# Performance work log

Measured on AMD Instinct MI355X. Metric: run time of the kernel, lower is better.

## Reference

```python
import jax, jax.numpy as jnp
import numpy as np

B, T, C = 2, 512, 128
H = 4 * C
EPS_LN = 1e-5
EPS_WKV = 1e-6


def setup_inputs() -> dict:
    key = jax.random.key(0)
    ks = jax.random.split(key, 12)
    def rn(i, shape, s):
        return jax.random.normal(ks[i], shape, jnp.float32) * s
    return {
        "x": jax.random.normal(ks[0], (B, T, C), jnp.float32),
        "ln1_g": jnp.ones((C,), jnp.float32), "ln1_b": jnp.zeros((C,), jnp.float32),
        "mu": rn(1, (C,), 0.1),
        "Wr": rn(2, (C, C), 0.02), "br": jnp.zeros((C,), jnp.float32),
        "Wk": rn(3, (C, C), 0.02), "bk": jnp.zeros((C,), jnp.float32),
        "Wv": rn(4, (C, C), 0.02), "bv": jnp.zeros((C,), jnp.float32),
        "w_decay": rn(5, (C,), 0.5),
        "Wo": rn(6, (C, C), 0.02), "bo": jnp.zeros((C,), jnp.float32),
        "ln2_g": jnp.ones((C,), jnp.float32), "ln2_b": jnp.zeros((C,), jnp.float32),
        "W1": rn(7, (C, H), 0.02), "b1": jnp.zeros((H,), jnp.float32),
        "W2": rn(8, (H, C), 0.02), "b2": jnp.zeros((C,), jnp.float32),
    }


def _ln(x, g, b):
    m = x.mean(-1, keepdims=True)
    v = ((x - m) ** 2).mean(-1, keepdims=True)
    return (x - m) * jax.lax.rsqrt(v + EPS_LN) * g + b


def _wkv_dir(k, v, w_lc):
    # k, v: (B,T,C); w_lc: (T,C) per-(position,channel) decay weight
    p = k[:, :, None, :] * w_lc[None, None, :, :]              # (B,T,L,C)
    p = jnp.exp(p - jax.lax.stop_gradient(p.max(-1, keepdims=True)))  # stable, max over C (as in source, dim=-1)
    p = p / (p.sum(-1, keepdims=True) + EPS_WKV)               # normalize over channel dim, as written in torch
    return jnp.einsum('btlc,blc->btc', p, v)


def _forward(x, ln1_g, ln1_b, mu, Wr, br, Wk, bk, Wv, bv, w_decay, Wo, bo, ln2_g, ln2_b, W1, b1, W2, b2):
    Tn = x.shape[1]
    h = _ln(x, ln1_g, ln1_b)
    # TemporalShift: past half shifted right, future half shifted left
    xp, xf = jnp.split(h, 2, axis=-1)
    xp = jnp.pad(xp, ((0, 0), (1, 0), (0, 0)))[:, :-1]
    xf = jnp.pad(xf, ((0, 0), (0, 1), (0, 0)))[:, 1:]
    hs = h + mu * jnp.concatenate([xp, xf], axis=-1)
    r = jax.nn.sigmoid(hs @ Wr + br)
    k = hs @ Wk + bk
    v = hs @ Wv + bv
    t = jnp.arange(Tn, dtype=x.dtype)[:, None]                 # (T,1)
    neg_w = -jnp.exp(w_decay)[None, :]                         # (1,C)
    w_f = neg_w * (Tn - 1 - t) / (Tn - 1)                      # (T,C)
    w_b = neg_w * t / (Tn - 1)                                 # (T,C)
    x_f = _wkv_dir(k, v, w_f)
    x_b = jnp.flip(_wkv_dir(jnp.flip(k, 1), jnp.flip(v, 1), w_b), 1)
    wk = r * (x_f + x_b) * 0.5
    y = x + wk @ Wo + bo
    h2 = _ln(y, ln2_g, ln2_b)
    m = jax.nn.gelu(h2 @ W1 + b1, approximate=False) @ W2 + b2
    return y + m


def reference(x, ln1_g, ln1_b, mu, Wr, br, Wk, bk, Wv, bv, w_decay, Wo, bo, ln2_g, ln2_b, W1, b1, W2, b2):
    return _forward(x, ln1_g, ln1_b, mu, Wr, br, Wk, bk, Wv, bv, w_decay, Wo, bo, ln2_g, ln2_b, W1, b1, W2, b2)
```

## Files before the change

### kernel.cpp

```cpp
#include <hip/hip_runtime.h>
#include <hip/hip_bf16.h>

#define Bq 2
#define Tq 512
#define Cq 128
#define Hq 512
#define NROW (Bq*Tq)

__device__ __forceinline__ float bfbits2f(unsigned short u) {
    return __uint_as_float(((unsigned)u) << 16);
}
__device__ __forceinline__ bool detect_f32(const void* sent) {
    return *(const unsigned*)sent == 0x3F800000u;
}
#define LD(p, i) (f32 ? ((const float*)(p))[i] : bfbits2f(((const unsigned short*)(p))[i]))
__device__ __forceinline__ float4 LD4(const void* p, int i, bool f32) {
    if (f32) return ((const float4*)p)[i >> 2];
    ushort4 u = *(const ushort4*)((const unsigned short*)p + i);
    return make_float4(bfbits2f(u.x), bfbits2f(u.y), bfbits2f(u.z), bfbits2f(u.w));
}

__global__ __launch_bounds__(512) void kA_qkv(
    const void* __restrict__ sent,
    const void* __restrict__ x,
    const void* __restrict__ ln1g, const void* __restrict__ ln1b,
    const void* __restrict__ mu,
    const void* __restrict__ Wr, const void* __restrict__ br,
    const void* __restrict__ Wk, const void* __restrict__ bk,
    const void* __restrict__ Wv, const void* __restrict__ bv,
    const void* __restrict__ wdec,
    float* __restrict__ r_out, float* __restrict__ u_out,
    float* __restrict__ v_out)
{
    const bool f32 = detect_f32(sent);
    int R0 = blockIdx.x * 2, tid = threadIdx.x;
    int g = tid >> 7, col = tid & 127;
    int t0 = R0 & (Tq - 1);
    int bbase = R0 - t0;

    __shared__ float h4[4][Cq];
    __shared__ __align__(16) float hsi[Cq][2];
    __shared__ __align__(16) float partA[3][2][2][Cq];
    __shared__ float wred[8][2];

    {
        int t = t0 - 1 + g;
        int tcl = min(max(t, 0), Tq - 1);
        int row = bbase + tcl;
        float xv = LD(x, row * Cq + col);
        float s1 = xv, s2 = xv * xv;
        for (int off = 32; off; off >>= 1) {
            s1 += __shfl_xor(s1, off);
            s2 += __shfl_xor(s2, off);
        }
        int wid = tid >> 6;
        if ((tid & 63) == 0) { wred[wid][0] = s1; wred[wid][1] = s2; }
        __syncthreads();
        float S1 = wred[2 * g][0] + wred[2 * g + 1][0];
        float S2 = wred[2 * g][1] + wred[2 * g + 1][1];
        float m  = S1 * (1.f / Cq);
        float va = S2 * (1.f / Cq) - m * m;
        float rs = rsqrtf(va + 1e-5f);
        h4[g][col] = (xv - m) * rs * LD(ln1g, col) + LD(ln1b, col);
    }
    __syncthreads();

    if (g < 2) {
        int r2 = g, tt = t0 + r2;
        float hv = h4[r2 + 1][col];
        float nb;
        if (col < Cq / 2) nb = (tt > 0)      ? h4[r2][col]     : 0.f;
        else              nb = (tt < Tq - 1) ? h4[r2 + 2][col] : 0.f;
        hsi[col][r2] = hv + LD(mu, col) * nb;
    }
    __syncthreads();

    {
        int w = tid >> 6, lane = tid & 63;
        if (w < 6) {
            int m = w >> 1, kh = w & 1;
            const void* W = (m == 0) ? Wr : (m == 1) ? Wk : Wv;
            int ks2 = lane >> 5, j0 = (lane & 31) * 4;
            int cbase = kh * 64 + ks2 * 32;
            float a00 = 0.f, a01 = 0.f, a02 = 0.f, a03 = 0.f;
            float a10 = 0.f, a11 = 0.f, a12 = 0.f, a13 = 0.f;
#pragma unroll 4
            for (int cc = cbase; cc < cbase + 32; ++cc) {
                float4 wv = LD4(W, cc * Cq + j0, f32);
                float2 hv = *(const float2*)&hsi[cc][0];
                a00 += hv.x * wv.x; a01 += hv.x * wv.y; a02 += hv.x * wv.z; a03 += hv.x * wv.w;
                a10 += hv.y * wv.x; a11 += hv.y * wv.y; a12 += hv.y * wv.z; a13 += hv.y * wv.w;
            }
            a00 += __shfl_xor(a00, 32);
            a01 += __shfl_xor(a01, 32);
            a02 += __shfl_xor(a02, 32);
            a03 += __shfl_xor(a03, 32);
            a10 += __shfl_xor(a10, 32);
            a11 += __shfl_xor(a11, 32);
            a12 += __shfl_xor(a12, 32);
            a13 += __shfl_xor(a13, 32);
            if (ks2 == 0) {
                *(float4*)&partA[m][kh][0][j0] = make_float4(a00, a01, a02, a03);
                *(float4*)&partA[m][kh][1][j0] = make_float4(a10, a11, a12, a13);
            }
        }
    }
    __syncthreads();

    if (g < 3) {
        int m = g;
        float ar0 = partA[m][0][0][col] + partA[m][1][0][col];
        float ar1 = partA[m][0][1][col] + partA[m][1][1][col];
        if (m == 0) {
            float bb = LD(br, col);
            r_out[(R0 + 0) * Cq + col] = 1.f / (1.f + __expf(-(ar0 + bb)));
            r_out[(R0 + 1) * Cq + col] = 1.f / (1.f + __expf(-(ar1 + bb)));
        } else if (m == 1) {
            float bb = LD(bk, col);
            float wd = LD(wdec, col);
            wd = fminf(fmaxf(wd, -20.f), 20.f);
            float negw = -__expf(wd);
            float u0 = (ar0 + bb) * negw;
            float u1 = (ar1 + bb) * negw;
            u0 = fminf(fmaxf(u0, -30.f), 30.f);
            u1 = fminf(fmaxf(u1, -30.f), 30.f);
            u_out[(R0 + 0) * Cq + col] = u0;
            u_out[(R0 + 1) * Cq + col] = u1;
        } else {
            float bb = LD(bv, col);
            v_out[(R0 + 0) * Cq + col] = ar0 + bb;
            v_out[(R0 + 1) * Cq + col] = ar1 + bb;
        }
    }
}

__global__ __launch_bounds__(512) void kB_wkv_ffn(
    const void* __restrict__ sent,
    const float* __restrict__ u_in,
    const float* __restrict__ v_in,
    const float* __restrict__ r_in,
    const void* __restrict__ x,
    const void* __restrict__ Wo, const void* __restrict__ bo,
    const void* __restrict__ lng, const void* __restrict__ lnb,
    const void* __restrict__ W1, const void* __restrict__ b1,
    const void* __restrict__ W2, const void* __restrict__ b2,
    void* __restrict__ out)
{
    const bool f32 = detect_f32(sent);
    int R0 = blockIdx.x * 2, tid = threadIdx.x;
    int b = R0 >> 9;
    const float inv511 = 1.f / (float)(Tq - 1);
    int w = tid >> 6, lane = tid & 63;

    __shared__ float u2[2][Cq];
    __shared__ __align__(16) float rinv2[Tq][2];
    __shared__ float part[8][2][Cq];
    __shared__ __align__(16) float wki[Cq][2];
    __shared__ __align__(16) float h2i[Cq][2];
    __shared__ __align__(16) float m1i[Hq][2];
    __shared__ __align__(16) float pbuf[16 * Cq * 2];
    __shared__ float wred[8][2];

    {
        const float4* us = (const float4*)(u_in + (size_t)R0 * Cq);
        ((float4*)u2)[lane] = us[lane];
    }
    float rv_pre = 0.f, xv_pre = 0.f;
    if (tid < 256) {
        int r = tid >> 7, c = tid & 127;
        rv_pre = r_in[(R0 + r) * Cq + c];
        xv_pre = LD(x, (R0 + r) * Cq + c);
    }

    {
        int l = (Tq - 1) - tid;
        float a = (float)tid * inv511 * 1.44269504f;
#pragma unroll
        for (int r = 0; r < 2; ++r) {
            float s0 = 0.f, s1 = 0.f, s2 = 0.f, s3 = 0.f;
            const float4* uu4 = (const float4*)u2[r];
            for (int cc = 0; cc < Cq / 4; ++cc) {
                float4 uv = uu4[cc];
                s0 += exp2f(a * uv.x);
                s1 += exp2f(a * uv.y);
                s2 += exp2f(a * uv.z);
                s3 += exp2f(a * uv.w);
            }
            rinv2[l][r] = 1.f / ((s0 + s1) + (s2 + s3) + 1e-6f);
        }
    }

    {
        int c2 = lane * 2;
        float u00 = u2[0][c2], u01 = u2[0][c2 + 1];
        float u10 = u2[1][c2], u11 = u2[1][c2 + 1];
        int j0 = w * 64;
        float jb = (float)j0;
        float e00 = __expf(u00 * jb * inv511), e01 = __expf(u01 * jb * inv511);
        float e10 = __expf(u10 * jb * inv511), e11 = __expf(u11 * jb * inv511);
        float g00 = __expf(u00 * inv511), g01 = __expf(u01 * inv511);
        float g10 = __expf(u10 * inv511), g11 = __expf(u11 * inv511);
        float a00 = 0.f, a01 = 0.f, a10 = 0.f, a11 = 0.f;
        int lhi = (Tq - 1) - j0;
        const float2* vp = (const float2*)(v_in + (size_t)b * Tq * Cq) + lane + (size_t)lhi * 64;
        const float2* rp = (const float2*)rinv2 + lhi;
        float2 v0 = vp[0], v1 = vp[-64], v2 = vp[-128], v3 = vp[-192];

#define WKV_QUAD(r0_, r1_, r2_, r3_)                                          \
        {                                                                     \
            { float f1 = e00 * g00, f2 = f1 * g00, f3 = f2 * g00;             \
              a00 += v0.x * (e00 * r0_.x);                                    \
              a00 += v1.x * (f1 * r1_.x);                                     \
              a00 += v2.x * (f2 * r2_.x);                                     \
              a00 += v3.x * (f3 * r3_.x);                                     \
              e00 = f3 * g00; }                                               \
            { float f1 = e01 * g01, f2 = f1 * g01, f3 = f2 * g01;             \
              a01 += v0.y * (e01 * r0_.x);                                    \
              a01 += v1.y * (f1 * r1_.x);                                    \
              a01 += v2.y * (f2 * r2_.x);                                    \
              a01 += v3.y * (f3 * r3_.x);                                    \
              e01 = f3 * g01; }                                               \
            { float f1 = e10 * g10, f2 = f1 * g10, f3 = f2 * g10;             \
              a10 += v0.x * (e10 * r0_.y);                                    \
              a10 += v1.x * (f1 * r1_.y);                                    \
              a10 += v2.x * (f2 * r2_.y);                                    \
              a10 += v3.x * (f3 * r3_.y);                                    \
              e10 = f3 * g10; }                                               \
            { float f1 = e11 * g11, f2 = f1 * g11, f3 = f2 * g11;             \
              a11 += v0.y * (e11 * r0_.y);                                    \
              a11 += v1.y * (f1 * r1_.y);                                    \
              a11 += v2.y * (f2 * r2_.y);                                    \
              a11 += v3.y * (f3 * r3_.y);                                    \
              e11 = f3 * g11; }                                               \
        }

        for (int it = 0; it < 15; ++it) {
            vp -= 256;
            float2 n0 = vp[0], n1 = vp[-64], n2 = vp[-128], n3 = vp[-192];
            float2 r0 = rp[0], r1 = rp[-1], r2 = rp[-2], r3 = rp[-3];
            rp -= 4;
            WKV_QUAD(r0, r1, r2, r3);
            v0 = n0; v1 = n1; v2 = n2; v3 = n3;
        }
        {
            float2 r0 = rp[0], r1 = rp[-1], r2 = rp[-2], r3 = rp[-3];
            WKV_QUAD(r0, r1, r2, r3);
        }
#undef WKV_QUAD
        part[w][0][c2]     = a00;
        part[w][0][c2 + 1] = a01;
        part[w][1][c2]     = a10;
        part[w][1][c2 + 1] = a11;
    }
    __syncthreads();

    if (tid < 256) {
        int r = tid >> 7, c = tid & 127;
        float acc = ((part[0][r][c] + part[1][r][c]) + (part[2][r][c] + part[3][r][c]))
                  + ((part[4][r][c] + part[5][r][c]) + (part[6][r][c] + part[7][r][c]));
        wki[c][r] = rv_pre * acc;
    }
    __syncthreads();

    {
        int ks = tid >> 5, c0 = (tid & 31) * 4;
        float a00 = 0.f, a01 = 0.f, a02 = 0.f, a03 = 0.f;
        float a10 = 0.f, a11 = 0.f, a12 = 0.f, a13 = 0.f;
        int k0 = ks * 8;
#pragma unroll
        for (int cc = k0; cc < k0 + 8; ++cc) {
            float4 wv   = LD4(Wo, cc * Cq + c0, f32);
            float2 wk2 = *(const float2*)&wki[cc][0];
            a00 += wk2.x * wv.x; a01 += wk2.x * wv.y; a02 += wk2.x * wv.z; a03 += wk2.x * wv.w;
            a10 += wk2.y * wv.x; a11 += wk2.y * wv.y; a12 += wk2.y * wv.z; a13 += wk2.y * wv.w;
        }
        *(float4*)&pbuf[(ks * Cq + c0) * 2]     = make_float4(a00, a10, a01, a11);
        *(float4*)&pbuf[(ks * Cq + c0 + 2) * 2] = make_float4(a02, a12, a03, a13);
    }
    __syncthreads();

    float yv = 0.f;
    if (tid < 256) {
        int c = tid & 127;
        float s = 0.f;
#pragma unroll
        for (int ks = 0; ks < 16; ++ks) s += pbuf[(ks * Cq + c) * 2 + (tid >> 7)];
        yv = xv_pre + s + LD(bo, c);
    }
    {
        float s1 = yv, s2 = yv * yv;
        for (int off = 32; off; off >>= 1) {
            s1 += __shfl_xor(s1, off);
            s2 += __shfl_xor(s2, off);
        }
        int wid = tid >> 6;
        if ((tid & 63) == 0) { wred[wid][0] = s1; wred[wid][1] = s2; }
        __syncthreads();
        if (tid < 256) {
            int r = tid >> 7, c = tid & 127;
            float S1 = wred[2 * r][0] + wred[2 * r + 1][0];
            float S2 = wred[2 * r][1] + wred[2 * r + 1][1];
            float m  = S1 * (1.f / Cq);
            float va = S2 * (1.f / Cq) - m * m;
            float rs = rsqrtf(va + 1e-5f);
            h2i[c][r] = (yv - m) * rs * LD(lng, c) + LD(lnb, c);
        }
    }
    __syncthreads();

    {
        int ks = tid >> 7, j0 = (tid & 127) * 4;
        float a00 = 0.f, a01 = 0.f, a02 = 0.f, a03 = 0.f;
        float a10 = 0.f, a11 = 0.f, a12 = 0.f, a13 = 0.f;
        int c0 = ks * 32;
        float4 p0 = LD4(W1, (c0 + 0) * Hq + j0, f32);
        float4 p1 = LD4(W1, (c0 + 1) * Hq + j0, f32);
        float4 p2 = LD4(W1, (c0 + 2) * Hq + j0, f32);
        float4 p3 = LD4(W1, (c0 + 3) * Hq + j0, f32);
#pragma unroll
        for (int gq = 0; gq < 8; ++gq) {
            int cc = c0 + gq * 4;
            float4 n0, n1, n2, n3;
            if (gq < 7) {
                n0 = LD4(W1, (cc + 4) * Hq + j0, f32);
                n1 = LD4(W1, (cc + 5) * Hq + j0, f32);
                n2 = LD4(W1, (cc + 6) * Hq + j0, f32);
                n3 = LD4(W1, (cc + 7) * Hq + j0, f32);
            }
            float2 h0 = *(const float2*)&h2i[cc + 0][0];
            float2 h1 = *(const float2*)&h2i[cc + 1][0];
            float2 h2 = *(const float2*)&h2i[cc + 2][0];
            float2 h3 = *(const float2*)&h2i[cc + 3][0];
            a00 += h0.x * p0.x; a01 += h0.x * p0.y; a02 += h0.x * p0.z; a03 += h0.x * p0.w;
            a10 += h0.y * p0.x; a11 += h0.y * p0.y; a12 += h0.y * p0.z; a13 += h0.y * p0.w;
            a00 += h1.x * p1.x; a01 += h1.x * p1.y; a02 += h1.x * p1.z; a03 += h1.x * p1.w;
            a10 += h1.y * p1.x; a11 += h1.y * p1.y; a12 += h1.y * p1.z; a13 += h1.y * p1.w;
            a00 += h2.x * p2.x; a01 += h2.x * p2.y; a02 += h2.x * p2.z; a03 += h2.x * p2.w;
            a10 += h2.y * p2.x; a11 += h2.y * p2.y; a12 += h2.y * p2.z; a13 += h2.y * p2.w;
            a00 += h3.x * p3.x; a01 += h3.x * p3.y; a02 += h3.x * p3.z; a03 += h3.x * p3.w;
            a10 += h3.y * p3.x; a11 += h3.y * p3.y; a12 += h3.y * p3.z; a13 += h3.y * p3.w;
            if (gq < 7) { p0 = n0; p1 = n1; p2 = n2; p3 = n3; }
        }
        *(float4*)&pbuf[(ks * Hq + j0) * 2]     = make_float4(a00, a10, a01, a11);
        *(float4*)&pbuf[(ks * Hq + j0 + 2) * 2] = make_float4(a02, a12, a03, a13);
    }
    __syncthreads();
    {
        int j = tid;
        float bb = LD(b1, j);
        float x0 = ((pbuf[(0 * Hq + j) * 2]     + pbuf[(1 * Hq + j) * 2])
                  + (pbuf[(2 * Hq + j) * 2]     + pbuf[(3 * Hq + j) * 2])) + bb;
        float x1 = ((pbuf[(0 * Hq + j) * 2 + 1] + pbuf[(1 * Hq + j) * 2 + 1])
                  + (pbuf[(2 * Hq + j) * 2 + 1] + pbuf[(3 * Hq + j) * 2 + 1])) + bb;
        m1i[j][0] = 0.5f * x0 * (1.f + erff(x0 * 0.70710678f));
        m1i[j][1] = 0.5f * x1 * (1.f + erff(x1 * 0.70710678f));
    }
    __syncthreads();

    {
        int ks = tid >> 5, c0 = (tid & 31) * 4;
        float a00 = 0.f, a01 = 0.f, a02 = 0.f, a03 = 0.f;
        float a10 = 0.f, a11 = 0.f, a12 = 0.f, a13 = 0.f;
        int h0b = ks * 32;
        float4 p0 = LD4(W2, (h0b + 0) * Cq + c0, f32);
        float4 p1 = LD4(W2, (h0b + 1) * Cq + c0, f32);
        float4 p2 = LD4(W2, (h0b + 2) * Cq + c0, f32);
        float4 p3 = LD4(W2, (h0b + 3) * Cq + c0, f32);
#pragma unroll
        for (int gq = 0; gq < 8; ++gq) {
            int hh = h0b + gq * 4;
            float4 n0, n1, n2, n3;
            if (gq < 7) {
                n0 = LD4(W2, (hh + 4) * Cq + c0, f32);
                n1 = LD4(W2, (hh + 5) * Cq + c0, f32);
                n2 = LD4(W2, (hh + 6) * Cq + c0, f32);
                n3 = LD4(W2, (hh + 7) * Cq + c0, f32);
            }
            float2 m0 = *(const float2*)&m1i[hh + 0][0];
            float2 m1 = *(const float2*)&m1i[hh + 1][0];
            float2 m2 = *(const float2*)&m1i[hh + 2][0];
            float2 m3 = *(const float2*)&m1i[hh + 3][0];
            a00 += m0.x * p0.x; a01 += m0.x * p0.y; a02 += m0.x * p0.z; a03 += m0.x * p0.w;
            a10 += m0.y * p0.x; a11 += m0.y * p0.y; a12 += m0.y * p0.z; a13 += m0.y * p0.w;
            a00 += m1.x * p1.x; a01 += m1.x * p1.y; a02 += m1.x * p1.z; a03 += m1.x * p1.w;
            a10 += m1.y * p1.x; a11 += m1.y * p1.y; a12 += m1.y * p1.z; a13 += m1.y * p1.w;
            a00 += m2.x * p2.x; a01 += m2.x * p2.y; a02 += m2.x * p2.z; a03 += m2.x * p2.w;
            a10 += m2.y * p2.x; a11 += m2.y * p2.y; a12 += m2.y * p2.z; a13 += m2.y * p2.w;
            a00 += m3.x * p3.x; a01 += m3.x * p3.y; a02 += m3.x * p3.z; a03 += m3.x * p3.w;
            a10 += m3.y * p3.x; a11 += m3.y * p3.y; a12 += m3.y * p3.z; a13 += m3.y * p3.w;
            if (gq < 7) { p0 = n0; p1 = n1; p2 = n2; p3 = n3; }
        }
        __syncthreads();
        *(float4*)&pbuf[(ks * Cq + c0) * 2]     = make_float4(a00, a10, a01, a11);
        *(float4*)&pbuf[(ks * Cq + c0 + 2) * 2] = make_float4(a02, a12, a03, a13);
    }
    __syncthreads();
    if (tid < 256) {
        int r = tid >> 7, c = tid & 127;
        float s = 0.f;
#pragma unroll
        for (int ks = 0; ks < 16; ++ks) s += pbuf[(ks * Cq + c) * 2 + r];
        float val = yv + s + LD(b2, c);
        int idx = (R0 + r) * Cq + c;
        if (f32) ((float*)out)[idx] = val;
        else     ((__hip_bfloat16*)out)[idx] = __float2bfloat16(val);
    }
}

extern "C" void kernel_launch(void* const* d_in, const int* in_sizes, int n_in,
                              void* d_out, int out_size, void* d_ws, size_t ws_size,
                              hipStream_t stream)
{
    const void* x    = d_in[0];
    const void* ln1g = d_in[1];
    const void* ln1b = d_in[2];
    const void* mu   = d_in[3];
    const void* Wr   = d_in[4];
    const void* br   = d_in[5];
    const void* Wk   = d_in[6];
    const void* bk   = d_in[7];
    const void* Wv   = d_in[8];
    const void* bv   = d_in[9];
    const void* wdec = d_in[10];
    const void* Wo   = d_in[11];
    const void* bo   = d_in[12];
    const void* ln2g = d_in[13];
    const void* ln2b = d_in[14];
    const void* W1   = d_in[15];
    const void* b1   = d_in[16];
    const void* W2   = d_in[17];
    const void* b2   = d_in[18];

    float* ws = (float*)d_ws;
    float* u  = ws;
    float* r  = ws + 131072;
    float* v  = ws + 262144;

    kA_qkv<<<NROW / 2, 512, 0, stream>>>(ln1g, x, ln1g, ln1b, mu, Wr, br, Wk, bk, Wv, bv, wdec, r, u, v);
    kB_wkv_ffn<<<NROW / 2, 512, 0, stream>>>(ln1g, u, v, r, x, Wo, bo, ln2g, ln2b, W1, b1, W2, b2, d_out);
}
```

Measured before the change: 141.0 us.

## Fuse QKV and WKV/FFN kernels into one launch with grid-wide atomic barrier

Merges the two kernels into a single persistent kernel. An atomic counter acts as a grid barrier between the QKV projection phase and the WKV/FFN phase, and a memset resets the counter before each launch. This removes one kernel launch and its gap. The cost is a spin-wait barrier that needs all 512 blocks to be co-resident (launch_bounds 512,4), plus an extra memset call; if occupancy is not enough the kernel can deadlock.

```diff
diff --git a/kernel.cpp b/kernel.cpp
--- a/kernel.cpp
+++ b/kernel.cpp
@@ -6,6 +6,7 @@
 #define Cq 128
 #define Hq 512
 #define NROW (Bq*Tq)
+#define NBLK (NROW/2)
 
 __device__ __forceinline__ float bfbits2f(unsigned short u) {
     return __uint_as_float(((unsigned)u) << 16);
@@ -20,7 +21,7 @@
     return make_float4(bfbits2f(u.x), bfbits2f(u.y), bfbits2f(u.z), bfbits2f(u.w));
 }
 
-__global__ __launch_bounds__(512) void kA_qkv(
+__global__ __launch_bounds__(512, 4) void kAB(
     const void* __restrict__ sent,
     const void* __restrict__ x,
     const void* __restrict__ ln1g, const void* __restrict__ ln1b,
@@ -29,129 +30,24 @@
     const void* __restrict__ Wk, const void* __restrict__ bk,
     const void* __restrict__ Wv, const void* __restrict__ bv,
     const void* __restrict__ wdec,
-    float* __restrict__ r_out, float* __restrict__ u_out,
-    float* __restrict__ v_out)
+    const void* __restrict__ Wo, const void* __restrict__ bo,
+    const void* __restrict__ lng, const void* __restrict__ lnb,
+    const void* __restrict__ W1, const void* __restrict__ b1,
+    const void* __restrict__ W2, const void* __restrict__ b2,
+    float* __restrict__ r_ws, float* __restrict__ u_ws, float* __restrict__ v_ws,
+    unsigned* __restrict__ ctr,
+    void* __restrict__ out)
 {
     const bool f32 = detect_f32(sent);
     int R0 = blockIdx.x * 2, tid = threadIdx.x;
     int g = tid >> 7, col = tid & 127;
-    int t0 = R0 & (Tq - 1);
-    int bbase = R0 - t0;
+    const float inv511 = 1.f / (float)(Tq - 1);
+    int w = tid >> 6, lane = tid & 63;
 
     __shared__ float h4[4][Cq];
     __shared__ __align__(16) float hsi[Cq][2];
     __shared__ __align__(16) float partA[3][2][2][Cq];
-    __shared__ float wred[8][2];
-
-    {
-        int t = t0 - 1 + g;
-        int tcl = min(max(t, 0), Tq - 1);
-        int row = bbase + tcl;
-        float xv = LD(x, row * Cq + col);
-        float s1 = xv, s2 = xv * xv;
-        for (int off = 32; off; off >>= 1) {
-            s1 += __shfl_xor(s1, off);
-            s2 += __shfl_xor(s2, off);
-        }
-        int wid = tid >> 6;
-        if ((tid & 63) == 0) { wred[wid][0] = s1; wred[wid][1] = s2; }
-        __syncthreads();
-        float S1 = wred[2 * g][0] + wred[2 * g + 1][0];
-        float S2 = wred[2 * g][1] + wred[2 * g + 1][1];
-        float m  = S1 * (1.f / Cq);
-        float va = S2 * (1.f / Cq) - m * m;
-        float rs = rsqrtf(va + 1e-5f);
-        h4[g][col] = (xv - m) * rs * LD(ln1g, col) + LD(ln1b, col);
-    }
-    __syncthreads();
-
-    if (g < 2) {
-        int r2 = g, tt = t0 + r2;
-        float hv = h4[r2 + 1][col];
-        float nb;
-        if (col < Cq / 2) nb = (tt > 0)      ? h4[r2][col]     : 0.f;
-        else              nb = (tt < Tq - 1) ? h4[r2 + 2][col] : 0.f;
-        hsi[col][r2] = hv + LD(mu, col) * nb;
-    }
-    __syncthreads();
-
-    {
-        int w = tid >> 6, lane = tid & 63;
-        if (w < 6) {
-            int m = w >> 1, kh = w & 1;
-            const void* W = (m == 0) ? Wr : (m == 1) ? Wk : Wv;
-            int ks2 = lane >> 5, j0 = (lane & 31) * 4;
-            int cbase = kh * 64 + ks2 * 32;
-            float a00 = 0.f, a01 = 0.f, a02 = 0.f, a03 = 0.f;
-            float a10 = 0.f, a11 = 0.f, a12 = 0.f, a13 = 0.f;
-#pragma unroll 4
-            for (int cc = cbase; cc < cbase + 32; ++cc) {
-                float4 wv = LD4(W, cc * Cq + j0, f32);
-                float2 hv = *(const float2*)&hsi[cc][0];
-                a00 += hv.x * wv.x; a01 += hv.x * wv.y; a02 += hv.x * wv.z; a03 += hv.x * wv.w;
-                a10 += hv.y * wv.x; a11 += hv.y * wv.y; a12 += hv.y * wv.z; a13 += hv.y * wv.w;
-            }
-            a00 += __shfl_xor(a00, 32);
-            a01 += __shfl_xor(a01, 32);
-            a02 += __shfl_xor(a02, 32);
-            a03 += __shfl_xor(a03, 32);
-            a10 += __shfl_xor(a10, 32);
-            a11 += __shfl_xor(a11, 32);
-            a12 += __shfl_xor(a12, 32);
-            a13 += __shfl_xor(a13, 32);
-            if (ks2 == 0) {
-                *(float4*)&partA[m][kh][0][j0] = make_float4(a00, a01, a02, a03);
-                *(float4*)&partA[m][kh][1][j0] = make_float4(a10, a11, a12, a13);
-            }
-        }
-    }
-    __syncthreads();
-
-    if (g < 3) {
-        int m = g;
-        float ar0 = partA[m][0][0][col] + partA[m][1][0][col];
-        float ar1 = partA[m][0][1][col] + partA[m][1][1][col];
-        if (m == 0) {
-            float bb = LD(br, col);
-            r_out[(R0 + 0) * Cq + col] = 1.f / (1.f + __expf(-(ar0 + bb)));
-            r_out[(R0 + 1) * Cq + col] = 1.f / (1.f + __expf(-(ar1 + bb)));
-        } else if (m == 1) {
-            float bb = LD(bk, col);
-            float wd = LD(wdec, col);
-            wd = fminf(fmaxf(wd, -20.f), 20.f);
-            float negw = -__expf(wd);
-            float u0 = (ar0 + bb) * negw;
-            float u1 = (ar1 + bb) * negw;
-            u0 = fminf(fmaxf(u0, -30.f), 30.f);
-            u1 = fminf(fmaxf(u1, -30.f), 30.f);
-            u_out[(R0 + 0) * Cq + col] = u0;
-            u_out[(R0 + 1) * Cq + col] = u1;
-        } else {
-            float bb = LD(bv, col);
-            v_out[(R0 + 0) * Cq + col] = ar0 + bb;
-            v_out[(R0 + 1) * Cq + col] = ar1 + bb;
-        }
-    }
-}
-
-__global__ __launch_bounds__(512) void kB_wkv_ffn(
-    const void* __restrict__ sent,
-    const float* __restrict__ u_in,
-    const float* __restrict__ v_in,
-    const float* __restrict__ r_in,
-    const void* __restrict__ x,
-    const void* __restrict__ Wo, const void* __restrict__ bo,
-    const void* __restrict__ lng, const void* __restrict__ lnb,
-    const void* __restrict__ W1, const void* __restrict__ b1,
-    const void* __restrict__ W2, const void* __restrict__ b2,
-    void* __restrict__ out)
-{
-    const bool f32 = detect_f32(sent);
-    int R0 = blockIdx.x * 2, tid = threadIdx.x;
-    int b = R0 >> 9;
-    const float inv511 = 1.f / (float)(Tq - 1);
-    int w = tid >> 6, lane = tid & 63;
-
+    __shared__ float wredA[8][2];
     __shared__ float u2[2][Cq];
     __shared__ __align__(16) float rinv2[Tq][2];
     __shared__ float part[8][2][Cq];
@@ -159,251 +55,360 @@
     __shared__ __align__(16) float h2i[Cq][2];
     __shared__ __align__(16) float m1i[Hq][2];
     __shared__ __align__(16) float pbuf[16 * Cq * 2];
-    __shared__ float wred[8][2];
+    __shared__ float wredB[8][2];
 
     {
-        const float4* us = (const float4*)(u_in + (size_t)R0 * Cq);
-        ((float4*)u2)[lane] = us[lane];
-    }
-    float rv_pre = 0.f, xv_pre = 0.f;
-    if (tid < 256) {
-        int r = tid >> 7, c = tid & 127;
-        rv_pre = r_in[(R0 + r) * Cq + c];
-        xv_pre = LD(x, (R0 + r) * Cq + c);
-    }
-
-    {
-        int l = (Tq - 1) - tid;
-        float a = (float)tid * inv511 * 1.44269504f;
-#pragma unroll
-        for (int r = 0; r < 2; ++r) {
-            float s0 = 0.f, s1 = 0.f, s2 = 0.f, s3 = 0.f;
-            const float4* uu4 = (const float4*)u2[r];
-            for (int cc = 0; cc < Cq / 4; ++cc) {
-                float4 uv = uu4[cc];
-                s0 += exp2f(a * uv.x);
-                s1 += exp2f(a * uv.y);
-                s2 += exp2f(a * uv.z);
-                s3 += exp2f(a * uv.w);
-            }
-            rinv2[l][r] = 1.f / ((s0 + s1) + (s2 + s3) + 1e-6f);
-        }
-    }
-
-    {
-        int c2 = lane * 2;
-        float u00 = u2[0][c2], u01 = u2[0][c2 + 1];
-        float u10 = u2[1][c2], u11 = u2[1][c2 + 1];
-        int j0 = w * 64;
-        float jb = (float)j0;
-        float e00 = __expf(u00 * jb * inv511), e01 = __expf(u01 * jb * inv511);
-        float e10 = __expf(u10 * jb * inv511), e11 = __expf(u11 * jb * inv511);
-        float g00 = __expf(u00 * inv511), g01 = __expf(u01 * inv511);
-        float g10 = __expf(u10 * inv511), g11 = __expf(u11 * inv511);
-        float a00 = 0.f, a01 = 0.f, a10 = 0.f, a11 = 0.f;
-        int lhi = (Tq - 1) - j0;
-        const float2* vp = (const float2*)(v_in + (size_t)b * Tq * Cq) + lane + (size_t)lhi * 64;
-        const float2* rp = (const float2*)rinv2 + lhi;
-        float2 v0 = vp[0], v1 = vp[-64], v2 = vp[-128], v3 = vp[-192];
-
-#define WKV_QUAD(r0_, r1_, r2_, r3_)                                          \
-        {                                                                     \
-            { float f1 = e00 * g00, f2 = f1 * g00, f3 = f2 * g00;             \
-              a00 += v0.x * (e00 * r0_.x);                                    \
-              a00 += v1.x * (f1 * r1_.x);                                     \
-              a00 += v2.x * (f2 * r2_.x);                                     \
-              a00 += v3.x * (f3 * r3_.x);                                     \
-              e00 = f3 * g00; }                                               \
-            { float f1 = e01 * g01, f2 = f1 * g01, f3 = f2 * g01;             \
-              a01 += v0.y * (e01 * r0_.x);                                    \
-              a01 += v1.y * (f1 * r1_.x);                                    \
-              a01 += v2.y * (f2 * r2_.x);                                    \
-              a01 += v3.y * (f3 * r3_.x);                                    \
-              e01 = f3 * g01; }                                               \
-            { float f1 = e10 * g10, f2 = f1 * g10, f3 = f2 * g10;             \
-              a10 += v0.x * (e10 * r0_.y);                                    \
-              a10 += v1.x * (f1 * r1_.y);                                    \
-              a10 += v2.x * (f2 * r2_.y);                                    \
-              a10 += v3.x * (f3 * r3_.y);                                    \
-              e10 = f3 * g10; }                                               \
-            { float f1 = e11 * g11, f2 = f1 * g11, f3 = f2 * g11;             \
-              a11 += v0.y * (e11 * r0_.y);                                    \
-              a11 += v1.y * (f1 * r1_.y);                                    \
-              a11 += v2.y * (f2 * r2_.y);                                    \
-              a11 += v3.y * (f3 * r3_.y);                                    \
-              e11 = f3 * g11; }                                               \
-        }
-
-        for (int it = 0; it < 15; ++it) {
-            vp -= 256;
-            float2 n0 = vp[0], n1 = vp[-64], n2 = vp[-128], n3 = vp[-192];
-            float2 r0 = rp[0], r1 = rp[-1], r2 = rp[-2], r3 = rp[-3];
-            rp -= 4;
-            WKV_QUAD(r0, r1, r2, r3);
-            v0 = n0; v1 = n1; v2 = n2; v3 = n3;
-        }
-        {
-            float2 r0 = rp[0], r1 = rp[-1], r2 = rp[-2], r3 = rp[-3];
-            WKV_QUAD(r0, r1, r2, r3);
-        }
-#undef WKV_QUAD
-        part[w][0][c2]     = a00;
-        part[w][0][c2 + 1] = a01;
-        part[w][1][c2]     = a10;
-        part[w][1][c2 + 1] = a11;
-    }
-    __syncthreads();
-
-    if (tid < 256) {
-        int r = tid >> 7, c = tid & 127;
-        float acc = ((part[0][r][c] + part[1][r][c]) + (part[2][r][c] + part[3][r][c]))
-                  + ((part[4][r][c] + part[5][r][c]) + (part[6][r][c] + part[7][r][c]));
-        wki[c][r] = rv_pre * acc;
-    }
-    __syncthreads();
-
-    {
-        int ks = tid >> 5, c0 = (tid & 31) * 4;
-        float a00 = 0.f, a01 = 0.f, a02 = 0.f, a03 = 0.f;
-        float a10 = 0.f, a11 = 0.f, a12 = 0.f, a13 = 0.f;
-        int k0 = ks * 8;
-#pragma unroll
-        for (int cc = k0; cc < k0 + 8; ++cc) {
-            float4 wv   = LD4(Wo, cc * Cq + c0, f32);
-            float2 wk2 = *(const float2*)&wki[cc][0];
-            a00 += wk2.x * wv.x; a01 += wk2.x * wv.y; a02 += wk2.x * wv.z; a03 += wk2.x * wv.w;
-            a10 += wk2.y * wv.x; a11 += wk2.y * wv.y; a12 += wk2.y * wv.z; a13 += wk2.y * wv.w;
-        }
-        *(float4*)&pbuf[(ks * Cq + c0) * 2]     = make_float4(a00, a10, a01, a11);
-        *(float4*)&pbuf[(ks * Cq + c0 + 2) * 2] = make_float4(a02, a12, a03, a13);
-    }
-    __syncthreads();
-
-    float yv = 0.f;
-    if (tid < 256) {
-        int c = tid & 127;
-        float s = 0.f;
-#pragma unroll
-        for (int ks = 0; ks < 16; ++ks) s += pbuf[(ks * Cq + c) * 2 + (tid >> 7)];
-        yv = xv_pre + s + LD(bo, c);
-    }
-    {
-        float s1 = yv, s2 = yv * yv;
-        for (int off = 32; off; off >>= 1) {
-            s1 += __shfl_xor(s1, off);
-            s2 += __shfl_xor(s2, off);
-        }
-        int wid = tid >> 6;
-        if ((tid & 63) == 0) { wred[wid][0] = s1; wred[wid][1] = s2; }
-        __syncthreads();
-        if (tid < 256) {
-            int r = tid >> 7, c = tid & 127;
-            float S1 = wred[2 * r][0] + wred[2 * r + 1][0];
-            float S2 = wred[2 * r][1] + wred[2 * r + 1][1];
+        int t0 = R0 & (Tq - 1);
+        int bbase = R0 - t0;
+
+        {
+            int t = t0 - 1 + g;
+            int tcl = min(max(t, 0), Tq - 1);
+            int row = bbase + tcl;
+            float xv = LD(x, row * Cq + col);
+            float s1 = xv, s2 = xv * xv;
+            for (int off = 32; off; off >>= 1) {
+                s1 += __shfl_xor(s1, off);
+                s2 += __shfl_xor(s2, off);
+            }
+            int wid = tid >> 6;
+            if ((tid & 63) == 0) { wredA[wid][0] = s1; wredA[wid][1] = s2; }
+            __syncthreads();
+            float S1 = wredA[2 * g][0] + wredA[2 * g + 1][0];
+            float S2 = wredA[2 * g][1] + wredA[2 * g + 1][1];
             float m  = S1 * (1.f / Cq);
             float va = S2 * (1.f / Cq) - m * m;
             float rs = rsqrtf(va + 1e-5f);
-            h2i[c][r] = (yv - m) * rs * LD(lng, c) + LD(lnb, c);
+            h4[g][col] = (xv - m) * rs * LD(ln1g, col) + LD(ln1b, col);
+        }
+        __syncthreads();
+
+        if (g < 2) {
+            int r2 = g, tt = t0 + r2;
+            float hv = h4[r2 + 1][col];
+            float nb;
+            if (col < Cq / 2) nb = (tt > 0)      ? h4[r2][col]     : 0.f;
+            else              nb = (tt < Tq - 1) ? h4[r2 + 2][col] : 0.f;
+            hsi[col][r2] = hv + LD(mu, col) * nb;
+        }
+        __syncthreads();
+
+        {
+            if (w < 6) {
+                int m = w >> 1, kh = w & 1;
+                const void* W = (m == 0) ? Wr : (m == 1) ? Wk : Wv;
+                int ks2 = lane >> 5, j0 = (lane & 31) * 4;
+                int cbase = kh * 64 + ks2 * 32;
+                float a00 = 0.f, a01 = 0.f, a02 = 0.f, a03 = 0.f;
+                float a10 = 0.f, a11 = 0.f, a12 = 0.f, a13 = 0.f;
+#pragma unroll 4
+                for (int cc = cbase; cc < cbase + 32; ++cc) {
+                    float4 wv = LD4(W, cc * Cq + j0, f32);
+                    float2 hv = *(const float2*)&hsi[cc][0];
+                    a00 += hv.x * wv.x; a01 += hv.x * wv.y; a02 += hv.x * wv.z; a03 += hv.x * wv.w;
+                    a10 += hv.y * wv.x; a11 += hv.y * wv.y; a12 += hv.y * wv.z; a13 += hv.y * wv.w;
+                }
+                a00 += __shfl_xor(a00, 32);
+                a01 += __shfl_xor(a01, 32);
+                a02 += __shfl_xor(a02, 32);
+                a03 += __shfl_xor(a03, 32);
+                a10 += __shfl_xor(a10, 32);
+                a11 += __shfl_xor(a11, 32);
+                a12 += __shfl_xor(a12, 32);
+                a13 += __shfl_xor(a13, 32);
+                if (ks2 == 0) {
+                    *(float4*)&partA[m][kh][0][j0] = make_float4(a00, a01, a02, a03);
+                    *(float4*)&partA[m][kh][1][j0] = make_float4(a10, a11, a12, a13);
+                }
+            }
+        }
+        __syncthreads();
+
+        if (g < 3) {
+            int m = g;
+            float ar0 = partA[m][0][0][col] + partA[m][1][0][col];
+            float ar1 = partA[m][0][1][col] + partA[m][1][1][col];
+            if (m == 0) {
+                float bb = LD(br, col);
+                r_ws[(R0 + 0) * Cq + col] = 1.f / (1.f + __expf(-(ar0 + bb)));
+                r_ws[(R0 + 1) * Cq + col] = 1.f / (1.f + __expf(-(ar1 + bb)));
+            } else if (m == 1) {
+                float bb = LD(bk, col);
+                float wd = LD(wdec, col);
+                wd = fminf(fmaxf(wd, -20.f), 20.f);
+                float negw = -__expf(wd);
+                float u0 = (ar0 + bb) * negw;
+                float u1 = (ar1 + bb) * negw;
+                u0 = fminf(fmaxf(u0, -30.f), 30.f);
+                u1 = fminf(fmaxf(u1, -30.f), 30.f);
+                u_ws[(R0 + 0) * Cq + col] = u0;
+                u_ws[(R0 + 1) * Cq + col] = u1;
+            } else {
+                float bb = LD(bv, col);
+                v_ws[(R0 + 0) * Cq + col] = ar0 + bb;
+                v_ws[(R0 + 1) * Cq + col] = ar1 + bb;
+            }
+        }
+    }
+
+    __threadfence();
+    __syncthreads();
+    if (tid == 0) {
+        atomicAdd(ctr, 1u);
+        while (atomicAdd(ctr, 0u) < (unsigned)NBLK) {
+            __builtin_amdgcn_s_sleep(16);
         }
     }
     __syncthreads();
+    __threadfence();
 
     {
-        int ks = tid >> 7, j0 = (tid & 127) * 4;
-        float a00 = 0.f, a01 = 0.f, a02 = 0.f, a03 = 0.f;
-        float a10 = 0.f, a11 = 0.f, a12 = 0.f, a13 = 0.f;
-        int c0 = ks * 32;
-        float4 p0 = LD4(W1, (c0 + 0) * Hq + j0, f32);
-        float4 p1 = LD4(W1, (c0 + 1) * Hq + j0, f32);
-        float4 p2 = LD4(W1, (c0 + 2) * Hq + j0, f32);
-        float4 p3 = LD4(W1, (c0 + 3) * Hq + j0, f32);
-#pragma unroll
-        for (int gq = 0; gq < 8; ++gq) {
-            int cc = c0 + gq * 4;
-            float4 n0, n1, n2, n3;
-            if (gq < 7) {
-                n0 = LD4(W1, (cc + 4) * Hq + j0, f32);
-                n1 = LD4(W1, (cc + 5) * Hq + j0, f32);
-                n2 = LD4(W1, (cc + 6) * Hq + j0, f32);
-                n3 = LD4(W1, (cc + 7) * Hq + j0, f32);
-            }
-            float2 h0 = *(const float2*)&h2i[cc + 0][0];
-            float2 h1 = *(const float2*)&h2i[cc + 1][0];
-            float2 h2 = *(const float2*)&h2i[cc + 2][0];
-            float2 h3 = *(const float2*)&h2i[cc + 3][0];
-            a00 += h0.x * p0.x; a01 += h0.x * p0.y; a02 += h0.x * p0.z; a03 += h0.x * p0.w;
-            a10 += h0.y * p0.x; a11 += h0.y * p0.y; a12 += h0.y * p0.z; a13 += h0.y * p0.w;
-            a00 += h1.x * p1.x; a01 += h1.x * p1.y; a02 += h1.x * p1.z; a03 += h1.x * p1.w;
-            a10 += h1.y * p1.x; a11 += h1.y * p1.y; a12 += h1.y * p1.z; a13 += h1.y * p1.w;
-            a00 += h2.x * p2.x; a01 += h2.x * p2.y; a02 += h2.x * p2.z; a03 += h2.x * p2.w;
-            a10 += h2.y * p2.x; a11 += h2.y * p2.y; a12 += h2.y * p2.z; a13 += h2.y * p2.w;
-            a00 += h3.x * p3.x; a01 += h3.x * p3.y; a02 += h3.x * p3.z; a03 += h3.x * p3.w;
-            a10 += h3.y * p3.x; a11 += h3.y * p3.y; a12 += h3.y * p3.z; a13 += h3.y * p3.w;
-            if (gq < 7) { p0 = n0; p1 = n1; p2 = n2; p3 = n3; }
-        }
-        *(float4*)&pbuf[(ks * Hq + j0) * 2]     = make_float4(a00, a10, a01, a11);
-        *(float4*)&pbuf[(ks * Hq + j0 + 2) * 2] = make_float4(a02, a12, a03, a13);
-    }
-    __syncthreads();
-    {
-        int j = tid;
-        float bb = LD(b1, j);
-        float x0 = ((pbuf[(0 * Hq + j) * 2]     + pbuf[(1 * Hq + j) * 2])
-                  + (pbuf[(2 * Hq + j) * 2]     + pbuf[(3 * Hq + j) * 2])) + bb;
-        float x1 = ((pbuf[(0 * Hq + j) * 2 + 1] + pbuf[(1 * Hq + j) * 2 + 1])
-                  + (pbuf[(2 * Hq + j) * 2 + 1] + pbuf[(3 * Hq + j) * 2 + 1])) + bb;
-        m1i[j][0] = 0.5f * x0 * (1.f + erff(x0 * 0.70710678f));
-        m1i[j][1] = 0.5f * x1 * (1.f + erff(x1 * 0.70710678f));
-    }
-    __syncthreads();
-
-    {
-        int ks = tid >> 5, c0 = (tid & 31) * 4;
-        float a00 = 0.f, a01 = 0.f, a02 = 0.f, a03 = 0.f;
-        float a10 = 0.f, a11 = 0.f, a12 = 0.f, a13 = 0.f;
-        int h0b = ks * 32;
-        float4 p0 = LD4(W2, (h0b + 0) * Cq + c0, f32);
-        float4 p1 = LD4(W2, (h0b + 1) * Cq + c0, f32);
-        float4 p2 = LD4(W2, (h0b + 2) * Cq + c0, f32);
-        float4 p3 = LD4(W2, (h0b + 3) * Cq + c0, f32);
-#pragma unroll
-        for (int gq = 0; gq < 8; ++gq) {
-            int hh = h0b + gq * 4;
-            float4 n0, n1, n2, n3;
-            if (gq < 7) {
-                n0 = LD4(W2, (hh + 4) * Cq + c0, f32);
-                n1 = LD4(W2, (hh + 5) * Cq + c0, f32);
-                n2 = LD4(W2, (hh + 6) * Cq + c0, f32);
-                n3 = LD4(W2, (hh + 7) * Cq + c0, f32);
-            }
-            float2 m0 = *(const float2*)&m1i[hh + 0][0];
-            float2 m1 = *(const float2*)&m1i[hh + 1][0];
-            float2 m2 = *(const float2*)&m1i[hh + 2][0];
-            float2 m3 = *(const float2*)&m1i[hh + 3][0];
-            a00 += m0.x * p0.x; a01 += m0.x * p0.y; a02 += m0.x * p0.z; a03 += m0.x * p0.w;
-            a10 += m0.y * p0.x; a11 += m0.y * p0.y; a12 += m0.y * p0.z; a13 += m0.y * p0.w;
-            a00 += m1.x * p1.x; a01 += m1.x * p1.y; a02 += m1.x * p1.z; a03 += m1.x * p1.w;
-            a10 += m1.y * p1.x; a11 += m1.y * p1.y; a12 += m1.y * p1.z; a13 += m1.y * p1.w;
-            a00 += m2.x * p2.x; a01 += m2.x * p2.y; a02 += m2.x * p2.z; a03 += m2.x * p2.w;
-            a10 += m2.y * p2.x; a11 += m2.y * p2.y; a12 += m2.y * p2.z; a13 += m2.y * p2.w;
-            a00 += m3.x * p3.x; a01 += m3.x * p3.y; a02 += m3.x * p3.z; a03 += m3.x * p3.w;
-            a10 += m3.y * p3.x; a11 += m3.y * p3.y; a12 += m3.y * p3.z; a13 += m3.y * p3.w;
-            if (gq < 7) { p0 = n0; p1 = n1; p2 = n2; p3 = n3; }
-        }
-        __syncthreads();
-        *(float4*)&pbuf[(ks * Cq + c0) * 2]     = make_float4(a00, a10, a01, a11);
-        *(float4*)&pbuf[(ks * Cq + c0 + 2) * 2] = make_float4(a02, a12, a03, a13);
-    }
-    __syncthreads();
-    if (tid < 256) {
-        int r = tid >> 7, c = tid & 127;
-        float s = 0.f;
-#pragma unroll
-        for (int ks = 0; ks < 16; ++ks) s += pbuf[(ks * Cq + c) * 2 + r];
-        float val = yv + s + LD(b2, c);
-        int idx = (R0 + r) * Cq + c;
-        if (f32) ((float*)out)[idx] = val;
-        else     ((__hip_bfloat16*)out)[idx] = __float2bfloat16(val);
+        int b = R0 >> 9;
+
+        {
+            const float4* us = (const float4*)(u_ws + (size_t)R0 * Cq);
+            ((float4*)u2)[lane] = us[lane];
+        }
+        float rv_pre = 0.f, xv_pre = 0.f;
+        if (tid < 256) {
+            int r = tid >> 7, c = tid & 127;
+            rv_pre = r_ws[(R0 + r) * Cq + c];
+            xv_pre = LD(x, (R0 + r) * Cq + c);
+        }
+
+        {
+            int l = (Tq - 1) - tid;
+            float a = (float)tid * inv511 * 1.44269504f;
+#pragma unroll
+            for (int r = 0; r < 2; ++r) {
+                float s0 = 0.f, s1 = 0.f, s2 = 0.f, s3 = 0.f;
+                const float4* uu4 = (const float4*)u2[r];
+                for (int cc = 0; cc < Cq / 4; ++cc) {
+                    float4 uv = uu4[cc];
+                    s0 += exp2f(a * uv.x);
+                    s1 += exp2f(a * uv.y);
+                    s2 += exp2f(a * uv.z);
+                    s3 += exp2f(a * uv.w);
+                }
+                rinv2[l][r] = 1.f / ((s0 + s1) + (s2 + s3) + 1e-6f);
+            }
+        }
+
+        {
+            int c2 = lane * 2;
+            float u00 = u2[0][c2], u01 = u2[0][c2 + 1];
+            float u10 = u2[1][c2], u11 = u2[1][c2 + 1];
+            int j0 = w * 64;
+            float jb = (float)j0;
+            float e00 = __expf(u00 * jb * inv511), e01 = __expf(u01 * jb * inv511);
+            float e10 = __expf(u10 * jb * inv511), e11 = __expf(u11 * jb * inv511);
+            float g00 = __expf(u00 * inv511), g01 = __expf(u01 * inv511);
+            float g10 = __expf(u10 * inv511), g11 = __expf(u11 * inv511);
+            float a00 = 0.f, a01 = 0.f, a10 = 0.f, a11 = 0.f;
+            int lhi = (Tq - 1) - j0;
+            const float2* vp = (const float2*)(v_ws + (size_t)b * Tq * Cq) + lane + (size_t)lhi * 64;
+            const float2* rp = (const float2*)rinv2 + lhi;
+            float2 v0 = vp[0], v1 = vp[-64], v2 = vp[-128], v3 = vp[-192];
+
+#define WKV_QUAD(r0_, r1_, r2_, r3_)                                          \
+            {                                                                 \
+                { float f1 = e00 * g00, f2 = f1 * g00, f3 = f2 * g00;         \
+                  a00 += v0.x * (e00 * r0_.x);                                \
+                  a00 += v1.x * (f1 * r1_.x);                                 \
+                  a00 += v2.x * (f2 * r2_.x);                                 \
+                  a00 += v3.x * (f3 * r3_.x);                                 \
+                  e00 = f3 * g00; }                                           \
+                { float f1 = e01 * g01, f2 = f1 * g01, f3 = f2 * g01;         \
+                  a01 += v0.y * (e01 * r0_.x);                                \
+                  a01 += v1.y * (f1 * r1_.x);                                 \
+                  a01 += v2.y * (f2 * r2_.x);                                 \
+                  a01 += v3.y * (f3 * r3_.x);                                 \
+                  e01 = f3 * g01; }                                           \
+                { float f1 = e10 * g10, f2 = f1 * g10, f3 = f2 * g10;         \
+                  a10 += v0.x * (e10 * r0_.y);                                \
+                  a10 += v1.x * (f1 * r1_.y);                                 \
+                  a10 += v2.x * (f2 * r2_.y);                                 \
+                  a10 += v3.x * (f3 * r3_.y);                                 \
+                  e10 = f3 * g10; }                                           \
+                { float f1 = e11 * g11, f2 = f1 * g11, f3 = f2 * g11;         \
+                  a11 += v0.y * (e11 * r0_.y);                                \
+                  a11 += v1.y * (f1 * r1_.y);                                 \
+                  a11 += v2.y * (f2 * r2_.y);                                 \
+                  a11 += v3.y * (f3 * r3_.y);                                 \
+                  e11 = f3 * g11; }                                           \
+            }
+
+            for (int it = 0; it < 15; ++it) {
+                vp -= 256;
+                float2 n0 = vp[0], n1 = vp[-64], n2 = vp[-128], n3 = vp[-192];
+                float2 r0 = rp[0], r1 = rp[-1], r2 = rp[-2], r3 = rp[-3];
+                rp -= 4;
+                WKV_QUAD(r0, r1, r2, r3);
+                v0 = n0; v1 = n1; v2 = n2; v3 = n3;
+            }
+            {
+                float2 r0 = rp[0], r1 = rp[-1], r2 = rp[-2], r3 = rp[-3];
+                WKV_QUAD(r0, r1, r2, r3);
+            }
+#undef WKV_QUAD
+            part[w][0][c2]     = a00;
+            part[w][0][c2 + 1] = a01;
+            part[w][1][c2]     = a10;
+            part[w][1][c2 + 1] = a11;
+        }
+        __syncthreads();
+
+        if (tid < 256) {
+            int r = tid >> 7, c = tid & 127;
+            float acc = ((part[0][r][c] + part[1][r][c]) + (part[2][r][c] + part[3][r][c]))
+                      + ((part[4][r][c] + part[5][r][c]) + (part[6][r][c] + part[7][r][c]));
+            wki[c][r] = rv_pre * acc;
+        }
+        __syncthreads();
+
+        {
+            int ks = tid >> 5, c0 = (tid & 31) * 4;
+            float a00 = 0.f, a01 = 0.f, a02 = 0.f, a03 = 0.f;
+            float a10 = 0.f, a11 = 0.f, a12 = 0.f, a13 = 0.f;
+            int k0 = ks * 8;
+#pragma unroll
+            for (int cc = k0; cc < k0 + 8; ++cc) {
+                float4 wv   = LD4(Wo, cc * Cq + c0, f32);
+                float2 wk2 = *(const float2*)&wki[cc][0];
+                a00 += wk2.x * wv.x; a01 += wk2.x * wv.y; a02 += wk2.x * wv.z; a03 += wk2.x * wv.w;
+                a10 += wk2.y * wv.x; a11 += wk2.y * wv.y; a12 += wk2.y * wv.z; a13 += wk2.y * wv.w;
+            }
+            *(float4*)&pbuf[(ks * Cq + c0) * 2]     = make_float4(a00, a10, a01, a11);
+            *(float4*)&pbuf[(ks * Cq + c0 + 2) * 2] = make_float4(a02, a12, a03, a13);
+        }
+        __syncthreads();
+
+        float yv = 0.f;
+        if (tid < 256) {
+            int c = tid & 127;
+            float s = 0.f;
+#pragma unroll
+            for (int ks = 0; ks < 16; ++ks) s += pbuf[(ks * Cq + c) * 2 + (tid >> 7)];
+            yv = xv_pre + s + LD(bo, c);
+        }
+        {
+            float s1 = yv, s2 = yv * yv;
+            for (int off = 32; off; off >>= 1) {
+                s1 += __shfl_xor(s1, off);
+                s2 += __shfl_xor(s2, off);
+            }
+            int wid = tid >> 6;
+            if ((tid & 63) == 0) { wredB[wid][0] = s1; wredB[wid][1] = s2; }
+            __syncthreads();
+            if (tid < 256) {
+                int r = tid >> 7, c = tid & 127;
+                float S1 = wredB[2 * r][0] + wredB[2 * r + 1][0];
+                float S2 = wredB[2 * r][1] + wredB[2 * r + 1][1];
+                float m  = S1 * (1.f / Cq);
+                float va = S2 * (1.f / Cq) - m * m;
+                float rs = rsqrtf(va + 1e-5f);
+                h2i[c][r] = (yv - m) * rs * LD(lng, c) + LD(lnb, c);
+            }
+        }
+        __syncthreads();
+
+        {
+            int ks = tid >> 7, j0 = (tid & 127) * 4;
+            float a00 = 0.f, a01 = 0.f, a02 = 0.f, a03 = 0.f;
+            float a10 = 0.f, a11 = 0.f, a12 = 0.f, a13 = 0.f;
+            int c0 = ks * 32;
+            float4 p0 = LD4(W1, (c0 + 0) * Hq + j0, f32);
+            float4 p1 = LD4(W1, (c0 + 1) * Hq + j0, f32);
+            float4 p2 = LD4(W1, (c0 + 2) * Hq + j0, f32);
+            float4 p3 = LD4(W1, (c0 + 3) * Hq + j0, f32);
+#pragma unroll
+            for (int gq = 0; gq < 8; ++gq) {
+                int cc = c0 + gq * 4;
+                float4 n0, n1, n2, n3;
+                if (gq < 7) {
+                    n0 = LD4(W1, (cc + 4) * Hq + j0, f32);
+                    n1 = LD4(W1, (cc + 5) * Hq + j0, f32);
+                    n2 = LD4(W1, (cc + 6) * Hq + j0, f32);
+                    n3 = LD4(W1, (cc + 7) * Hq + j0, f32);
+                }
+                float2 h0 = *(const float2*)&h2i[cc + 0][0];
+                float2 h1 = *(const float2*)&h2i[cc + 1][0];
+                float2 h2 = *(const float2*)&h2i[cc + 2][0];
+                float2 h3 = *(const float2*)&h2i[cc + 3][0];
+                a00 += h0.x * p0.x; a01 += h0.x * p0.y; a02 += h0.x * p0.z; a03 += h0.x * p0.w;
+                a10 += h0.y * p0.x; a11 += h0.y * p0.y; a12 += h0.y * p0.z; a13 += h0.y * p0.w;
+                a00 += h1.x * p1.x; a01 += h1.x * p1.y; a02 += h1.x * p1.z; a03 += h1.x * p1.w;
+                a10 += h1.y * p1.x; a11 += h1.y * p1.y; a12 += h1.y * p1.z; a13 += h1.y * p1.w;
+                a00 += h2.x * p2.x; a01 += h2.x * p2.y; a02 += h2.x * p2.z; a03 += h2.x * p2.w;
+                a10 += h2.y * p2.x; a11 += h2.y * p2.y; a12 += h2.y * p2.z; a13 += h2.y * p2.w;
+                a00 += h3.x * p3.x; a01 += h3.x * p3.y; a02 += h3.x * p3.z; a03 += h3.x * p3.w;
+                a10 += h3.y * p3.x; a11 += h3.y * p3.y; a12 += h3.y * p3.z; a13 += h3.y * p3.w;
+                if (gq < 7) { p0 = n0; p1 = n1; p2 = n2; p3 = n3; }
+            }
+            *(float4*)&pbuf[(ks * Hq + j0) * 2]     = make_float4(a00, a10, a01, a11);
+            *(float4*)&pbuf[(ks * Hq + j0 + 2) * 2] = make_float4(a02, a12, a03, a13);
+        }
+        __syncthreads();
+        {
+            int j = tid;
+            float bb = LD(b1, j);
+            float x0 = ((pbuf[(0 * Hq + j) * 2]     + pbuf[(1 * Hq + j) * 2])
+                      + (pbuf[(2 * Hq + j) * 2]     + pbuf[(3 * Hq + j) * 2])) + bb;
+            float x1 = ((pbuf[(0 * Hq + j) * 2 + 1] + pbuf[(1 * Hq + j) * 2 + 1])
+                      + (pbuf[(2 * Hq + j) * 2 + 1] + pbuf[(3 * Hq + j) * 2 + 1])) + bb;
+            m1i[j][0] = 0.5f * x0 * (1.f + erff(x0 * 0.70710678f));
+            m1i[j][1] = 0.5f * x1 * (1.f + erff(x1 * 0.70710678f));
+        }
+        __syncthreads();
+
+        {
+            int ks = tid >> 5, c0 = (tid & 31) * 4;
+            float a00 = 0.f, a01 = 0.f, a02 = 0.f, a03 = 0.f;
+            float a10 = 0.f, a11 = 0.f, a12 = 0.f, a13 = 0.f;
+            int h0b = ks * 32;
+            float4 p0 = LD4(W2, (h0b + 0) * Cq + c0, f32);
+            float4 p1 = LD4(W2, (h0b + 1) * Cq + c0, f32);
+            float4 p2 = LD4(W2, (h0b + 2) * Cq + c0, f32);
+            float4 p3 = LD4(W2, (h0b + 3) * Cq + c0, f32);
+#pragma unroll
+            for (int gq = 0; gq < 8; ++gq) {
+                int hh = h0b + gq * 4;
+                float4 n0, n1, n2, n3;
+                if (gq < 7) {
+                    n0 = LD4(W2, (hh + 4) * Cq + c0, f32);
+                    n1 = LD4(W2, (hh + 5) * Cq + c0, f32);
+                    n2 = LD4(W2, (hh + 6) * Cq + c0, f32);
+                    n3 = LD4(W2, (hh + 7) * Cq + c0, f32);
+                }
+                float2 m0 = *(const float2*)&m1i[hh + 0][0];
+                float2 m1 = *(const float2*)&m1i[hh + 1][0];
+                float2 m2 = *(const float2*)&m1i[hh + 2][0];
+                float2 m3 = *(const float2*)&m1i[hh + 3][0];
+                a00 += m0.x * p0.x; a01 += m0.x * p0.y; a02 += m0.x * p0.z; a03 += m0.x * p0.w;
+                a10 += m0.y * p0.x; a11 += m0.y * p0.y; a12 += m0.y * p0.z; a13 += m0.y * p0.w;
+                a00 += m1.x * p1.x; a01 += m1.x * p1.y; a02 += m1.x * p1.z; a03 += m1.x * p1.w;
+                a10 += m1.y * p1.x; a11 += m1.y * p1.y; a12 += m1.y * p1.z; a13 += m1.y * p1.w;
+                a00 += m2.x * p2.x; a01 += m2.x * p2.y; a02 += m2.x * p2.z; a03 += m2.x * p2.w;
+                a10 += m2.y * p2.x; a11 += m2.y * p2.y; a12 += m2.y * p2.z; a13 += m2.y * p2.w;
+                a00 += m3.x * p3.x; a01 += m3.x * p3.y; a02 += m3.x * p3.z; a03 += m3.x * p3.w;
+                a10 += m3.y * p3.x; a11 += m3.y * p3.y; a12 += m3.y * p3.z; a13 += m3.y * p3.w;
+                if (gq < 7) { p0 = n0; p1 = n1; p2 = n2; p3 = n3; }
+            }
+            __syncthreads();
+            *(float4*)&pbuf[(ks * Cq + c0) * 2]     = make_float4(a00, a10, a01, a11);
+            *(float4*)&pbuf[(ks * Cq + c0 + 2) * 2] = make_float4(a02, a12, a03, a13);
+        }
+        __syncthreads();
+        if (tid < 256) {
+            int r = tid >> 7, c = tid & 127;
+            float s = 0.f;
+#pragma unroll
+            for (int ks = 0; ks < 16; ++ks) s += pbuf[(ks * Cq + c) * 2 + r];
+            float val = yv + s + LD(b2, c);
+            int idx = (R0 + r) * Cq + c;
+            if (f32) ((float*)out)[idx] = val;
+            else     ((__hip_bfloat16*)out)[idx] = __float2bfloat16(val);
+        }
     }
 }
 
@@ -435,7 +440,11 @@
     float* u  = ws;
     float* r  = ws + 131072;
     float* v  = ws + 262144;
-
-    kA_qkv<<<NROW / 2, 512, 0, stream>>>(ln1g, x, ln1g, ln1b, mu, Wr, br, Wk, bk, Wv, bv, wdec, r, u, v);
-    kB_wkv_ffn<<<NROW / 2, 512, 0, stream>>>(ln1g, u, v, r, x, Wo, bo, ln2g, ln2b, W1, b1, W2, b2, d_out);
+    unsigned* ctr = (unsigned*)(ws + 393216);
+
+    hipMemsetAsync((void*)ctr, 0, sizeof(unsigned), stream);
+    kAB<<<NBLK, 512, 0, stream>>>(ln1g, x, ln1g, ln1b, mu,
+                                  Wr, br, Wk, bk, Wv, bv, wdec,
+                                  Wo, bo, ln2g, ln2b, W1, b1, W2, b2,
+                                  r, u, v, ctr, d_out);
 }
```

Measured after the change: 371.4 us. 2.63x slower.
